# Kernel tuning notes

Hardware: AMD Instinct MI355X
Metric: run time of the kernel (lower is better)

Reference implementation:

```python
import jax, jax.numpy as jnp
import numpy as np

TEMPERATURE = 0.5
EPS = 1e-12  # matches torch F.normalize eps

def setup_inputs() -> dict:
    key = jax.random.key(0)
    k1, k2, k3 = jax.random.split(key, 3)
    B, D = 4096, 256
    return {
        "query": jax.random.normal(k1, (B, D), dtype=jnp.float32),
        "pos": jax.random.normal(k2, (B, D), dtype=jnp.float32),
        "neg": jax.random.normal(k3, (B, D), dtype=jnp.float32),
    }

def _l2norm(x):
    n = jnp.maximum(jnp.linalg.norm(x, axis=1, keepdims=True), EPS)
    return x / n

def reference(query, pos, neg):
    B = query.shape[0]
    z_q = _l2norm(query)
    z_p = _l2norm(pos)
    # neg is normalized in the original but never used in the loss
    z = jnp.concatenate([z_q, z_p], axis=0)           # [2B, D]
    # cosine similarity of unit vectors == dot product -> single matmul
    sim = z @ z.T                                      # [2B, 2B]
    sim_ij = jnp.diagonal(sim, offset=B)               # [B]
    sim_ji = jnp.diagonal(sim, offset=-B)              # [B]
    positives = jnp.concatenate([sim_ij, sim_ji])      # [2B]
    mask = 1.0 - jnp.eye(2 * B, dtype=sim.dtype)       # negatives_mask
    denom = jnp.sum(mask * jnp.exp(sim / TEMPERATURE), axis=1)  # [2B]
    loss_partial = -(positives / TEMPERATURE - jnp.log(denom))
    return jnp.sum(loss_partial) / (2 * B)
```

## Files before the change

### kernel.cpp

```cpp
#include <hip/hip_runtime.h>
#include <hip/hip_bf16.h>
#include <math.h>

#define B_ROWS 4096
#define D_DIM  256
#define N_TOT  8192
#define E2     7.38905609893065f
#define NTILE  64
#define NBLK   (NTILE * (NTILE + 1) / 2)

typedef __attribute__((ext_vector_type(4))) float f32x4;
typedef __attribute__((ext_vector_type(8))) short bf16x8;

__device__ __forceinline__ void async_copy16(const void* gptr, void* lptr) {
    __builtin_amdgcn_global_load_lds(
        (const __attribute__((address_space(1))) unsigned int*)gptr,
        (__attribute__((address_space(3))) unsigned int*)lptr,
        16 , 0 , 0 );
}

__global__ __launch_bounds__(256) void norm_kernel(
        const float* __restrict__ q, const float* __restrict__ p,
        __hip_bfloat16* __restrict__ Z, float* __restrict__ pospart,
        float* __restrict__ denom) {
    const int row = blockIdx.x;
    const int t   = threadIdx.x;
    if (row < 32) denom[row * 256 + t] = 0.0f;
    const float qv = q[row * D_DIM + t];
    const float pv = p[row * D_DIM + t];
    float a = qv * qv, b = pv * pv, c = qv * pv;
    #pragma unroll
    for (int off = 32; off > 0; off >>= 1) {
        a += __shfl_down(a, off);
        b += __shfl_down(b, off);
        c += __shfl_down(c, off);
    }
    __shared__ float red[3][4];
    const int wv = t >> 6, ln = t & 63;
    if (ln == 0) { red[0][wv] = a; red[1][wv] = b; red[2][wv] = c; }
    __syncthreads();
    const float nq  = red[0][0] + red[0][1] + red[0][2] + red[0][3];
    const float np2 = red[1][0] + red[1][1] + red[1][2] + red[1][3];
    const float qp  = red[2][0] + red[2][1] + red[2][2] + red[2][3];
    const float rq = 1.0f / fmaxf(sqrtf(nq),  1e-12f);
    const float rp = 1.0f / fmaxf(sqrtf(np2), 1e-12f);
    Z[(size_t)row * D_DIM + t]            = __float2bfloat16(qv * rq);
    Z[(size_t)(B_ROWS + row) * D_DIM + t] = __float2bfloat16(pv * rp);
    if (t == 0) pospart[row] = qp * rq * rp;
}

__global__ __launch_bounds__(256, 3) void simexp_gemm(
        const __hip_bfloat16* __restrict__ Z, float* __restrict__ denom) {
    __shared__ __hip_bfloat16 As[128 * 64];
    __shared__ __hip_bfloat16 Bs[128 * 64];
    const int tid    = threadIdx.x;
    const int lane   = tid & 63;
    const int wv     = tid >> 6;
    const int wave_m = wv >> 1;
    const int wave_n = wv & 1;
    const int m16    = lane & 15;
    const int quad   = lane >> 4;

    const int bid = blockIdx.x;
    int bi = (int)((129.0 - sqrt(129.0 * 129.0 - 8.0 * (double)bid)) * 0.5);
    while (bi > 0 && (bi * NTILE - bi * (bi - 1) / 2) > bid) --bi;
    while (((bi + 1) * NTILE - (bi + 1) * bi / 2) <= bid) ++bi;
    const int bj = bi + (bid - (bi * NTILE - bi * (bi - 1) / 2));
    const int rowBase = bi * 128;
    const int colBase = bj * 128;

    f32x4 acc[4][4];
    #pragma unroll
    for (int i = 0; i < 4; ++i)
        #pragma unroll
        for (int j = 0; j < 4; ++j) acc[i][j] = (f32x4){0.f, 0.f, 0.f, 0.f};

    const int lrow = lane >> 3;
    const int lchk = lane & 7;

    for (int kt = 0; kt < 4; ++kt) {
        const int k0 = kt * 64;
        __syncthreads();
        #pragma unroll
        for (int pp = 0; pp < 4; ++pp) {
            const int r = wv * 32 + pp * 8 + lrow;
            const int g = lchk ^ (r & 7);
            const __hip_bfloat16* srcA =
                Z + (size_t)(rowBase + r) * D_DIM + k0 + g * 8;
            const __hip_bfloat16* srcB =
                Z + (size_t)(colBase + r) * D_DIM + k0 + g * 8;
            async_copy16(srcA, (char*)As + (wv * 32 + pp * 8) * 128);
            async_copy16(srcB, (char*)Bs + (wv * 32 + pp * 8) * 128);
        }
        __syncthreads();

        #pragma unroll
        for (int kt2 = 0; kt2 < 2; ++kt2) {
            const int sw = (kt2 * 4 + quad) ^ (m16 & 7);
            bf16x8 af[4], bfr[4];
            #pragma unroll
            for (int mi = 0; mi < 4; ++mi) {
                const int r = wave_m * 64 + mi * 16 + m16;
                af[mi] = *(const bf16x8*)((const char*)As + r * 128 + sw * 16);
            }
            #pragma unroll
            for (int ni = 0; ni < 4; ++ni) {
                const int r = wave_n * 64 + ni * 16 + m16;
                bfr[ni] = *(const bf16x8*)((const char*)Bs + r * 128 + sw * 16);
            }
            #pragma unroll
            for (int mi = 0; mi < 4; ++mi)
                #pragma unroll
                for (int ni = 0; ni < 4; ++ni)
                    acc[mi][ni] = __builtin_amdgcn_mfma_f32_16x16x32_bf16(
                        af[mi], bfr[ni], acc[mi][ni], 0, 0, 0);
        }
    }

    float cs[4] = {0.f, 0.f, 0.f, 0.f};
    float rs[4][4];
    #pragma unroll
    for (int mi = 0; mi < 4; ++mi)
        #pragma unroll
        for (int r = 0; r < 4; ++r) {
            float s = 0.f;
            #pragma unroll
            for (int ni = 0; ni < 4; ++ni) {
                const float e = __expf(2.0f * acc[mi][ni][r]);
                s += e;
                cs[ni] += e;
            }
            rs[mi][r] = s;
        }
    #pragma unroll
    for (int off = 1; off < 16; off <<= 1)
        #pragma unroll
        for (int mi = 0; mi < 4; ++mi)
            #pragma unroll
            for (int r = 0; r < 4; ++r)
                rs[mi][r] += __shfl_xor(rs[mi][r], off, 64);
    if (m16 == 0) {
        #pragma unroll
        for (int mi = 0; mi < 4; ++mi)
            #pragma unroll
            for (int r = 0; r < 4; ++r)
                atomicAdd(&denom[rowBase + wave_m * 64 + mi * 16 + quad * 4 + r],
                          rs[mi][r]);
    }
    if (bi != bj) {
        #pragma unroll
        for (int off = 16; off < 64; off <<= 1)
            #pragma unroll
            for (int ni = 0; ni < 4; ++ni)
                cs[ni] += __shfl_xor(cs[ni], off, 64);
        if (lane < 16) {
            #pragma unroll
            for (int ni = 0; ni < 4; ++ni)
                atomicAdd(&denom[colBase + wave_n * 64 + ni * 16 + m16], cs[ni]);
        }
    }
}

__global__ __launch_bounds__(256) void finalize_kernel(
        const float* __restrict__ denom, const float* __restrict__ pospart,
        float* __restrict__ out) {
    const int t = threadIdx.x;
    float s = 0.f;
    for (int i = t; i < N_TOT; i += 256) s += logf(denom[i] - E2);
    float pp = 0.f;
    for (int i = t; i < B_ROWS; i += 256) pp += pospart[i];
    s -= 4.0f * pp;
    #pragma unroll
    for (int off = 32; off > 0; off >>= 1) s += __shfl_down(s, off);
    __shared__ float red[4];
    if ((t & 63) == 0) red[t >> 6] = s;
    __syncthreads();
    if (t == 0)
        out[0] = (red[0] + red[1] + red[2] + red[3]) / (float)N_TOT;
}

extern "C" void kernel_launch(void* const* d_in, const int* in_sizes, int n_in,
                              void* d_out, int out_size, void* d_ws, size_t ws_size,
                              hipStream_t stream) {
    const float* q = (const float*)d_in[0];
    const float* p = (const float*)d_in[1];
    float* out = (float*)d_out;

    __hip_bfloat16* Z = (__hip_bfloat16*)d_ws;
    float* denom   = (float*)((char*)d_ws + (size_t)N_TOT * D_DIM * sizeof(__hip_bfloat16));
    float* pospart = denom + N_TOT;

    hipLaunchKernelGGL(norm_kernel, dim3(B_ROWS), dim3(256), 0, stream,
                       q, p, Z, pospart, denom);
    hipLaunchKernelGGL(simexp_gemm, dim3(NBLK), dim3(256), 0, stream, Z, denom);
    hipLaunchKernelGGL(finalize_kernel, dim3(1), dim3(256), 0, stream,
                       denom, pospart, out);
}
```

Baseline: 118.3 us.

## Replace LDS-tiled symmetric GEMM with per-wave 64x64 tiles loading directly from global

Each wave now owns one 64x64 tile of the upper-triangular similarity matrix and reads its bf16 fragments straight from global memory, with no shared-memory staging and no block barriers. This removes LDS traffic and __syncthreads stalls, and the finer tile grid lets the triangular work balance better across many more waves. In exchange, reuse across waves inside a block is lost, so total global/L2 reads roughly double, and the per-lane loads are strided 16-byte accesses that rely on the cache. There are also twice as many atomics on denom because the diagonal tiles are smaller.

Measured after the change: 169.5 us. 43.4% more time.

```diff
diff --git a/kernel.cpp b/kernel.cpp
--- a/kernel.cpp
+++ b/kernel.cpp
@@ -6,18 +6,13 @@
 #define D_DIM  256
 #define N_TOT  8192
 #define E2     7.38905609893065f
-#define NTILE  64
-#define NBLK   (NTILE * (NTILE + 1) / 2)
+#define NT64   128
+#define NPAIR  (NT64 * (NT64 + 1) / 2)
+#define WPB    4
+#define NBLK2  (NPAIR / WPB)
 
 typedef __attribute__((ext_vector_type(4))) float f32x4;
 typedef __attribute__((ext_vector_type(8))) short bf16x8;
-
-__device__ __forceinline__ void async_copy16(const void* gptr, void* lptr) {
-    __builtin_amdgcn_global_load_lds(
-        (const __attribute__((address_space(1))) unsigned int*)gptr,
-        (__attribute__((address_space(3))) unsigned int*)lptr,
-        16 , 0 , 0 );
-}
 
 __global__ __launch_bounds__(256) void norm_kernel(
         const float* __restrict__ q, const float* __restrict__ p,
@@ -49,25 +44,30 @@
     if (t == 0) pospart[row] = qp * rq * rp;
 }
 
-__global__ __launch_bounds__(256, 3) void simexp_gemm(
+__global__ __launch_bounds__(256, 4) void simexp_direct(
         const __hip_bfloat16* __restrict__ Z, float* __restrict__ denom) {
-    __shared__ __hip_bfloat16 As[128 * 64];
-    __shared__ __hip_bfloat16 Bs[128 * 64];
-    const int tid    = threadIdx.x;
-    const int lane   = tid & 63;
-    const int wv     = tid >> 6;
-    const int wave_m = wv >> 1;
-    const int wave_n = wv & 1;
-    const int m16    = lane & 15;
-    const int quad   = lane >> 4;
+    const int tid  = threadIdx.x;
+    const int lane = tid & 63;
+    const int wv   = tid >> 6;
+    const int m16  = lane & 15;
+    const int quad = lane >> 4;
 
-    const int bid = blockIdx.x;
-    int bi = (int)((129.0 - sqrt(129.0 * 129.0 - 8.0 * (double)bid)) * 0.5);
-    while (bi > 0 && (bi * NTILE - bi * (bi - 1) / 2) > bid) --bi;
-    while (((bi + 1) * NTILE - (bi + 1) * bi / 2) <= bid) ++bi;
-    const int bj = bi + (bid - (bi * NTILE - bi * (bi - 1) / 2));
-    const int rowBase = bi * 128;
-    const int colBase = bj * 128;
+    const int gw = blockIdx.x * WPB + wv;
+
+    int bi = (int)((257.0 - sqrt(257.0 * 257.0 - 8.0 * (double)gw)) * 0.5);
+    while (bi > 0 && (bi * NT64 - bi * (bi - 1) / 2) > gw) --bi;
+    while (((bi + 1) * NT64 - (bi + 1) * bi / 2) <= gw) ++bi;
+    const int bj = bi + (gw - (bi * NT64 - bi * (bi - 1) / 2));
+    const int rowBase = bi * 64;
+    const int colBase = bj * 64;
+
+    const __hip_bfloat16* abase[4];
+    const __hip_bfloat16* bbase[4];
+    #pragma unroll
+    for (int i = 0; i < 4; ++i) {
+        abase[i] = Z + (size_t)(rowBase + i * 16 + m16) * D_DIM + quad * 8;
+        bbase[i] = Z + (size_t)(colBase + i * 16 + m16) * D_DIM + quad * 8;
+    }
 
     f32x4 acc[4][4];
     #pragma unroll
@@ -75,46 +75,21 @@
         #pragma unroll
         for (int j = 0; j < 4; ++j) acc[i][j] = (f32x4){0.f, 0.f, 0.f, 0.f};
 
-    const int lrow = lane >> 3;
-    const int lchk = lane & 7;
-
-    for (int kt = 0; kt < 4; ++kt) {
-        const int k0 = kt * 64;
-        __syncthreads();
+    #pragma unroll
+    for (int kk = 0; kk < 8; ++kk) {
+        bf16x8 af[4], bfr[4];
         #pragma unroll
-        for (int pp = 0; pp < 4; ++pp) {
-            const int r = wv * 32 + pp * 8 + lrow;
-            const int g = lchk ^ (r & 7);
-            const __hip_bfloat16* srcA =
-                Z + (size_t)(rowBase + r) * D_DIM + k0 + g * 8;
-            const __hip_bfloat16* srcB =
-                Z + (size_t)(colBase + r) * D_DIM + k0 + g * 8;
-            async_copy16(srcA, (char*)As + (wv * 32 + pp * 8) * 128);
-            async_copy16(srcB, (char*)Bs + (wv * 32 + pp * 8) * 128);
-        }
-        __syncthreads();
-
+        for (int i = 0; i < 4; ++i)
+            af[i] = *(const bf16x8*)(abase[i] + kk * 32);
         #pragma unroll
-        for (int kt2 = 0; kt2 < 2; ++kt2) {
-            const int sw = (kt2 * 4 + quad) ^ (m16 & 7);
-            bf16x8 af[4], bfr[4];
+        for (int i = 0; i < 4; ++i)
+            bfr[i] = *(const bf16x8*)(bbase[i] + kk * 32);
+        #pragma unroll
+        for (int mi = 0; mi < 4; ++mi)
             #pragma unroll
-            for (int mi = 0; mi < 4; ++mi) {
-                const int r = wave_m * 64 + mi * 16 + m16;
-                af[mi] = *(const bf16x8*)((const char*)As + r * 128 + sw * 16);
-            }
-            #pragma unroll
-            for (int ni = 0; ni < 4; ++ni) {
-                const int r = wave_n * 64 + ni * 16 + m16;
-                bfr[ni] = *(const bf16x8*)((const char*)Bs + r * 128 + sw * 16);
-            }
-            #pragma unroll
-            for (int mi = 0; mi < 4; ++mi)
-                #pragma unroll
-                for (int ni = 0; ni < 4; ++ni)
-                    acc[mi][ni] = __builtin_amdgcn_mfma_f32_16x16x32_bf16(
-                        af[mi], bfr[ni], acc[mi][ni], 0, 0, 0);
-        }
+            for (int ni = 0; ni < 4; ++ni)
+                acc[mi][ni] = __builtin_amdgcn_mfma_f32_16x16x32_bf16(
+                    af[mi], bfr[ni], acc[mi][ni], 0, 0, 0);
     }
 
     float cs[4] = {0.f, 0.f, 0.f, 0.f};
@@ -144,8 +119,7 @@
         for (int mi = 0; mi < 4; ++mi)
             #pragma unroll
             for (int r = 0; r < 4; ++r)
-                atomicAdd(&denom[rowBase + wave_m * 64 + mi * 16 + quad * 4 + r],
-                          rs[mi][r]);
+                atomicAdd(&denom[rowBase + mi * 16 + quad * 4 + r], rs[mi][r]);
     }
     if (bi != bj) {
         #pragma unroll
@@ -156,7 +130,7 @@
         if (lane < 16) {
             #pragma unroll
             for (int ni = 0; ni < 4; ++ni)
-                atomicAdd(&denom[colBase + wave_n * 64 + ni * 16 + m16], cs[ni]);
+                atomicAdd(&denom[colBase + ni * 16 + m16], cs[ni]);
         }
     }
 }
@@ -192,7 +166,7 @@
 
     hipLaunchKernelGGL(norm_kernel, dim3(B_ROWS), dim3(256), 0, stream,
                        q, p, Z, pospart, denom);
-    hipLaunchKernelGGL(simexp_gemm, dim3(NBLK), dim3(256), 0, stream, Z, denom);
+    hipLaunchKernelGGL(simexp_direct, dim3(NBLK2), dim3(256), 0, stream, Z, denom);
     hipLaunchKernelGGL(finalize_kernel, dim3(1), dim3(256), 0, stream,
                        denom, pospart, out);
 }
```

## Use 8 waves per GEMM block with 64x32 per-wave tiles and precomputed load offsets

Applied to the files above, without the earlier changes.

The symmetric sim-exp GEMM block grows from 4 to 8 waves (512 threads), arranged 2x4, so each wave computes a 64x32 sub-tile instead of 64x64. This halves accumulator registers per wave and splits the async LDS loads across more waves, aiming to add latency hiding and occupancy. Global load offsets are now computed once and advanced per K step, and LDS addressing uses constant strides. In exchange, A fragments are re-read from LDS by more waves and there are more atomics per block for row sums.

After: 148.2 us. 1.25x slower.

```diff
diff --git a/kernel.cpp b/kernel.cpp
--- a/kernel.cpp
+++ b/kernel.cpp
@@ -49,15 +49,15 @@
     if (t == 0) pospart[row] = qp * rq * rp;
 }
 
-__global__ __launch_bounds__(256, 3) void simexp_gemm(
+__global__ __launch_bounds__(512) void simexp_gemm(
         const __hip_bfloat16* __restrict__ Z, float* __restrict__ denom) {
     __shared__ __hip_bfloat16 As[128 * 64];
     __shared__ __hip_bfloat16 Bs[128 * 64];
     const int tid    = threadIdx.x;
     const int lane   = tid & 63;
     const int wv     = tid >> 6;
-    const int wave_m = wv >> 1;
-    const int wave_n = wv & 1;
+    const int wave_m = wv >> 2;
+    const int wave_n = wv & 3;
     const int m16    = lane & 15;
     const int quad   = lane >> 4;
 
@@ -69,55 +69,60 @@
     const int rowBase = bi * 128;
     const int colBase = bj * 128;
 
-    f32x4 acc[4][4];
+    f32x4 acc[4][2];
     #pragma unroll
     for (int i = 0; i < 4; ++i)
         #pragma unroll
-        for (int j = 0; j < 4; ++j) acc[i][j] = (f32x4){0.f, 0.f, 0.f, 0.f};
+        for (int j = 0; j < 2; ++j) acc[i][j] = (f32x4){0.f, 0.f, 0.f, 0.f};
 
     const int lrow = lane >> 3;
     const int lchk = lane & 7;
+    unsigned int aoff[2], boff[2];
+    #pragma unroll
+    for (int pp = 0; pp < 2; ++pp) {
+        const int r = wv * 16 + pp * 8 + lrow;
+        const int g = lchk ^ (r & 7);
+        aoff[pp] = (unsigned int)((rowBase + r) * 512 + g * 16);
+        boff[pp] = (unsigned int)((colBase + r) * 512 + g * 16);
+    }
 
     for (int kt = 0; kt < 4; ++kt) {
-        const int k0 = kt * 64;
         __syncthreads();
         #pragma unroll
-        for (int pp = 0; pp < 4; ++pp) {
-            const int r = wv * 32 + pp * 8 + lrow;
-            const int g = lchk ^ (r & 7);
-            const __hip_bfloat16* srcA =
-                Z + (size_t)(rowBase + r) * D_DIM + k0 + g * 8;
-            const __hip_bfloat16* srcB =
-                Z + (size_t)(colBase + r) * D_DIM + k0 + g * 8;
-            async_copy16(srcA, (char*)As + (wv * 32 + pp * 8) * 128);
-            async_copy16(srcB, (char*)Bs + (wv * 32 + pp * 8) * 128);
+        for (int pp = 0; pp < 2; ++pp) {
+            async_copy16((const char*)Z + aoff[pp],
+                         (char*)As + (wv * 16 + pp * 8) * 128);
+            async_copy16((const char*)Z + boff[pp],
+                         (char*)Bs + (wv * 16 + pp * 8) * 128);
+            aoff[pp] += 128;
+            boff[pp] += 128;
         }
         __syncthreads();
 
         #pragma unroll
         for (int kt2 = 0; kt2 < 2; ++kt2) {
             const int sw = (kt2 * 4 + quad) ^ (m16 & 7);
-            bf16x8 af[4], bfr[4];
-            #pragma unroll
-            for (int mi = 0; mi < 4; ++mi) {
-                const int r = wave_m * 64 + mi * 16 + m16;
-                af[mi] = *(const bf16x8*)((const char*)As + r * 128 + sw * 16);
-            }
-            #pragma unroll
-            for (int ni = 0; ni < 4; ++ni) {
-                const int r = wave_n * 64 + ni * 16 + m16;
-                bfr[ni] = *(const bf16x8*)((const char*)Bs + r * 128 + sw * 16);
-            }
+            const unsigned int abase =
+                (unsigned int)((wave_m * 64 + m16) * 128 + sw * 16);
+            const unsigned int bbase =
+                (unsigned int)((wave_n * 32 + m16) * 128 + sw * 16);
+            bf16x8 af[4], bfr[2];
+            #pragma unroll
+            for (int mi = 0; mi < 4; ++mi)
+                af[mi] = *(const bf16x8*)((const char*)As + abase + mi * 2048);
+            #pragma unroll
+            for (int ni = 0; ni < 2; ++ni)
+                bfr[ni] = *(const bf16x8*)((const char*)Bs + bbase + ni * 2048);
             #pragma unroll
             for (int mi = 0; mi < 4; ++mi)
                 #pragma unroll
-                for (int ni = 0; ni < 4; ++ni)
+                for (int ni = 0; ni < 2; ++ni)
                     acc[mi][ni] = __builtin_amdgcn_mfma_f32_16x16x32_bf16(
                         af[mi], bfr[ni], acc[mi][ni], 0, 0, 0);
         }
     }
 
-    float cs[4] = {0.f, 0.f, 0.f, 0.f};
+    float cs[2] = {0.f, 0.f};
     float rs[4][4];
     #pragma unroll
     for (int mi = 0; mi < 4; ++mi)
@@ -125,7 +130,7 @@
         for (int r = 0; r < 4; ++r) {
             float s = 0.f;
             #pragma unroll
-            for (int ni = 0; ni < 4; ++ni) {
+            for (int ni = 0; ni < 2; ++ni) {
                 const float e = __expf(2.0f * acc[mi][ni][r]);
                 s += e;
                 cs[ni] += e;
@@ -151,12 +156,12 @@
         #pragma unroll
         for (int off = 16; off < 64; off <<= 1)
             #pragma unroll
-            for (int ni = 0; ni < 4; ++ni)
+            for (int ni = 0; ni < 2; ++ni)
                 cs[ni] += __shfl_xor(cs[ni], off, 64);
         if (lane < 16) {
             #pragma unroll
-            for (int ni = 0; ni < 4; ++ni)
-                atomicAdd(&denom[colBase + wave_n * 64 + ni * 16 + m16], cs[ni]);
+            for (int ni = 0; ni < 2; ++ni)
+                atomicAdd(&denom[colBase + wave_n * 32 + ni * 16 + m16], cs[ni]);
         }
     }
 }
@@ -192,7 +197,7 @@
 
     hipLaunchKernelGGL(norm_kernel, dim3(B_ROWS), dim3(256), 0, stream,
                        q, p, Z, pospart, denom);
-    hipLaunchKernelGGL(simexp_gemm, dim3(NBLK), dim3(256), 0, stream, Z, denom);
+    hipLaunchKernelGGL(simexp_gemm, dim3(NBLK), dim3(512), 0, stream, Z, denom);
     hipLaunchKernelGGL(finalize_kernel, dim3(1), dim3(256), 0, stream,
                        denom, pospart, out);
 }
```

## Replace denominator atomics with per-slot partial buffer and separate reduce kernel

Applied to the files above, without the earlier changes.

Each GEMM tile now writes its row and column exp-sum partials to a dedicated slot in a 128x8192 partial buffer instead of calling atomicAdd on the shared denominator. A new reduce kernel sums the 128 slots per row, so the zeroing pass in the norm kernel goes away. Global and LDS load addresses are also precomputed and advanced incrementally, and the occupancy hint on the GEMM kernel is dropped. This removes atomic contention but adds an extra kernel launch and about 4 MB of partial-buffer traffic.

Result: slower. 121.1 us (+2.4%).

```diff
diff --git a/kernel.cpp b/kernel.cpp
--- a/kernel.cpp
+++ b/kernel.cpp
@@ -8,6 +8,7 @@
 #define E2     7.38905609893065f
 #define NTILE  64
 #define NBLK   (NTILE * (NTILE + 1) / 2)
+#define NSLOT  128
 
 typedef __attribute__((ext_vector_type(4))) float f32x4;
 typedef __attribute__((ext_vector_type(8))) short bf16x8;
@@ -21,11 +22,9 @@
 
 __global__ __launch_bounds__(256) void norm_kernel(
         const float* __restrict__ q, const float* __restrict__ p,
-        __hip_bfloat16* __restrict__ Z, float* __restrict__ pospart,
-        float* __restrict__ denom) {
+        __hip_bfloat16* __restrict__ Z, float* __restrict__ pospart) {
     const int row = blockIdx.x;
     const int t   = threadIdx.x;
-    if (row < 32) denom[row * 256 + t] = 0.0f;
     const float qv = q[row * D_DIM + t];
     const float pv = p[row * D_DIM + t];
     float a = qv * qv, b = pv * pv, c = qv * pv;
@@ -49,8 +48,8 @@
     if (t == 0) pospart[row] = qp * rq * rp;
 }
 
-__global__ __launch_bounds__(256, 3) void simexp_gemm(
-        const __hip_bfloat16* __restrict__ Z, float* __restrict__ denom) {
+__global__ __launch_bounds__(256) void simexp_gemm(
+        const __hip_bfloat16* __restrict__ Z, float* __restrict__ bufP) {
     __shared__ __hip_bfloat16 As[128 * 64];
     __shared__ __hip_bfloat16 Bs[128 * 64];
     const int tid    = threadIdx.x;
@@ -77,37 +76,42 @@
 
     const int lrow = lane >> 3;
     const int lchk = lane & 7;
+    unsigned int aoff[4], boff[4];
+    #pragma unroll
+    for (int pp = 0; pp < 4; ++pp) {
+        const int r = wv * 32 + pp * 8 + lrow;
+        const int g = lchk ^ (r & 7);
+        aoff[pp] = (unsigned int)((rowBase + r) * 512 + g * 16);
+        boff[pp] = (unsigned int)((colBase + r) * 512 + g * 16);
+    }
 
     for (int kt = 0; kt < 4; ++kt) {
-        const int k0 = kt * 64;
         __syncthreads();
         #pragma unroll
         for (int pp = 0; pp < 4; ++pp) {
-            const int r = wv * 32 + pp * 8 + lrow;
-            const int g = lchk ^ (r & 7);
-            const __hip_bfloat16* srcA =
-                Z + (size_t)(rowBase + r) * D_DIM + k0 + g * 8;
-            const __hip_bfloat16* srcB =
-                Z + (size_t)(colBase + r) * D_DIM + k0 + g * 8;
-            async_copy16(srcA, (char*)As + (wv * 32 + pp * 8) * 128);
-            async_copy16(srcB, (char*)Bs + (wv * 32 + pp * 8) * 128);
+            async_copy16((const char*)Z + aoff[pp],
+                         (char*)As + (wv * 32 + pp * 8) * 128);
+            async_copy16((const char*)Z + boff[pp],
+                         (char*)Bs + (wv * 32 + pp * 8) * 128);
+            aoff[pp] += 128;
+            boff[pp] += 128;
         }
         __syncthreads();
 
         #pragma unroll
         for (int kt2 = 0; kt2 < 2; ++kt2) {
             const int sw = (kt2 * 4 + quad) ^ (m16 & 7);
+            const unsigned int abase =
+                (unsigned int)((wave_m * 64 + m16) * 128 + sw * 16);
+            const unsigned int bbase =
+                (unsigned int)((wave_n * 64 + m16) * 128 + sw * 16);
             bf16x8 af[4], bfr[4];
             #pragma unroll
-            for (int mi = 0; mi < 4; ++mi) {
-                const int r = wave_m * 64 + mi * 16 + m16;
-                af[mi] = *(const bf16x8*)((const char*)As + r * 128 + sw * 16);
-            }
-            #pragma unroll
-            for (int ni = 0; ni < 4; ++ni) {
-                const int r = wave_n * 64 + ni * 16 + m16;
-                bfr[ni] = *(const bf16x8*)((const char*)Bs + r * 128 + sw * 16);
-            }
+            for (int mi = 0; mi < 4; ++mi)
+                af[mi] = *(const bf16x8*)((const char*)As + abase + mi * 2048);
+            #pragma unroll
+            for (int ni = 0; ni < 4; ++ni)
+                bfr[ni] = *(const bf16x8*)((const char*)Bs + bbase + ni * 2048);
             #pragma unroll
             for (int mi = 0; mi < 4; ++mi)
                 #pragma unroll
@@ -140,12 +144,12 @@
             for (int r = 0; r < 4; ++r)
                 rs[mi][r] += __shfl_xor(rs[mi][r], off, 64);
     if (m16 == 0) {
+        float* dst = bufP + (size_t)(2 * bj + wave_n) * N_TOT + rowBase;
         #pragma unroll
         for (int mi = 0; mi < 4; ++mi)
             #pragma unroll
             for (int r = 0; r < 4; ++r)
-                atomicAdd(&denom[rowBase + wave_m * 64 + mi * 16 + quad * 4 + r],
-                          rs[mi][r]);
+                dst[wave_m * 64 + mi * 16 + quad * 4 + r] = rs[mi][r];
     }
     if (bi != bj) {
         #pragma unroll
@@ -154,11 +158,26 @@
             for (int ni = 0; ni < 4; ++ni)
                 cs[ni] += __shfl_xor(cs[ni], off, 64);
         if (lane < 16) {
+            float* dst = bufP + (size_t)(2 * bi + wave_m) * N_TOT + colBase;
             #pragma unroll
             for (int ni = 0; ni < 4; ++ni)
-                atomicAdd(&denom[colBase + wave_n * 64 + ni * 16 + m16], cs[ni]);
-        }
-    }
+                dst[wave_n * 64 + ni * 16 + m16] = cs[ni];
+        }
+    }
+}
+
+__global__ __launch_bounds__(256) void reduce_kernel(
+        const float* __restrict__ bufP, float* __restrict__ denom) {
+    const int r = blockIdx.x * 256 + threadIdx.x;
+    float s0 = 0.f, s1 = 0.f, s2 = 0.f, s3 = 0.f;
+    #pragma unroll 4
+    for (int t = 0; t < NSLOT; t += 4) {
+        s0 += bufP[(size_t)(t + 0) * N_TOT + r];
+        s1 += bufP[(size_t)(t + 1) * N_TOT + r];
+        s2 += bufP[(size_t)(t + 2) * N_TOT + r];
+        s3 += bufP[(size_t)(t + 3) * N_TOT + r];
+    }
+    denom[r] = (s0 + s1) + (s2 + s3);
 }
 
 __global__ __launch_bounds__(256) void finalize_kernel(
@@ -187,12 +206,15 @@
     float* out = (float*)d_out;
 
     __hip_bfloat16* Z = (__hip_bfloat16*)d_ws;
-    float* denom   = (float*)((char*)d_ws + (size_t)N_TOT * D_DIM * sizeof(__hip_bfloat16));
+    float* bufP    = (float*)((char*)d_ws + (size_t)N_TOT * D_DIM * sizeof(__hip_bfloat16));
+    float* denom   = bufP + (size_t)NSLOT * N_TOT;
     float* pospart = denom + N_TOT;
 
     hipLaunchKernelGGL(norm_kernel, dim3(B_ROWS), dim3(256), 0, stream,
-                       q, p, Z, pospart, denom);
-    hipLaunchKernelGGL(simexp_gemm, dim3(NBLK), dim3(256), 0, stream, Z, denom);
+                       q, p, Z, pospart);
+    hipLaunchKernelGGL(simexp_gemm, dim3(NBLK), dim3(256), 0, stream, Z, bufP);
+    hipLaunchKernelGGL(reduce_kernel, dim3(N_TOT / 256), dim3(256), 0, stream,
+                       bufP, denom);
     hipLaunchKernelGGL(finalize_kernel, dim3(1), dim3(256), 0, stream,
                        denom, pospart, out);
 }
```
